# Optimization experiments

Hardware: AMD Instinct MI355X
Metric: run time of the kernel (lower is better)

The kernel has to match this reference:

```python
import jax, jax.numpy as jnp
import numpy as np

B = 131072
HID = 512
TEMB = 32
N_STEPS = 10


def time_embedding(t):
    # t: (B,) -> (B, TEMB) sinusoidal embedding
    half = TEMB // 2
    freqs = jnp.exp(-jnp.log(10000.0) * jnp.arange(half, dtype=jnp.float32) / half)
    args = t[:, None] * freqs[None, :]
    return jnp.concatenate([jnp.sin(args), jnp.cos(args)], axis=-1)


def setup_inputs() -> dict:
    key = jax.random.key(0)
    ks = jax.random.split(key, 9)
    def lin(k, fan_out, fan_in):
        s = 1.0 / np.sqrt(fan_in)
        kw, kb = jax.random.split(k)
        W = jax.random.uniform(kw, (fan_out, fan_in), jnp.float32, -s, s)
        b = jax.random.uniform(kb, (fan_out,), jnp.float32, -s, s)
        return W, b
    x = jax.random.normal(ks[0], (B, 2), jnp.float32)
    W0, b0 = lin(ks[1], HID, 2 + TEMB)
    W1, b1 = lin(ks[2], HID, HID)
    W2, b2 = lin(ks[3], HID, HID)
    # NOTE: original zero-inits last layer (trivial flow); use small random
    # weights so the Jacobian/log-det math is exercised non-trivially.
    W3 = 0.1 * jax.random.normal(ks[4], (2, HID), jnp.float32) / np.sqrt(HID)
    b3 = jnp.zeros((2,), jnp.float32)
    return {"x": x, "W0": W0, "b0": b0, "W1": W1, "b1": b1,
            "W2": W2, "b2": b2, "W3": W3, "b3": b3}


def reference(x, W0, b0, W1, b1, W2, b2, W3, b3):
    h_step = 1.0 / N_STEPS
    nb = x.shape[0]

    def vel(z, t):
        # z: (B,2), t: (B,) -> v: (B,2)
        h = jnp.concatenate([z, time_embedding(t)], axis=-1)
        h = jax.nn.silu(h @ W0.T + b0)
        h = jax.nn.silu(h @ W1.T + b1)
        h = jax.nn.silu(h @ W2.T + b2)
        return h @ W3.T + b3

    e0 = jnp.broadcast_to(jnp.array([1.0, 0.0], jnp.float32), (nb, 2))
    e1 = jnp.broadcast_to(jnp.array([0.0, 1.0], jnp.float32), (nb, 2))

    def step(carry, k):
        z, log_det = carry
        t = jnp.full((nb,), k * h_step, jnp.float32)
        f = lambda zz: vel(zz, t)
        # Batched JVPs give Jacobian columns: col0 = dv/dz0, col1 = dv/dz1
        v, col0 = jax.jvp(f, (z,), (e0,))
        _, col1 = jax.jvp(f, (z,), (e1,))
        det = (1.0 + h_step * col0[:, 0]) * (1.0 + h_step * col1[:, 1]) \
              - (h_step ** 2) * col1[:, 0] * col0[:, 1]
        log_det = log_det + jnp.log(jnp.clip(jnp.abs(det), 1e-8))
        z = z + h_step * v
        return (z, log_det), None

    ks = jnp.arange(N_STEPS, dtype=jnp.float32)
    (z, log_det), _ = jax.lax.scan(step, (x, jnp.zeros((nb,), jnp.float32)), ks)
    log_pz = -0.5 * jnp.sum(z ** 2 + jnp.log(2.0 * jnp.pi), axis=-1)
    return log_pz + log_det
```

## Files before the change

### kernel.cpp

```cpp
#include <hip/hip_runtime.h>
#include <hip/hip_bf16.h>
#include <math.h>


typedef float  f32x4  __attribute__((ext_vector_type(4)));
typedef float  f32x16 __attribute__((ext_vector_type(16)));
typedef __bf16 bf16x8 __attribute__((ext_vector_type(8)));

#define ROWB(r) (((r) << 10) + ((r) << 4))

static __device__ __forceinline__ unsigned pkbf2(float a, float b) {
    unsigned short lo = __builtin_bit_cast(unsigned short, __float2bfloat16(a));
    unsigned short hi = __builtin_bit_cast(unsigned short, __float2bfloat16(b));
    return (unsigned)lo | ((unsigned)hi << 16);
}

__global__ void pack_w_kernel(const float* __restrict__ W,
                              __hip_bfloat16* __restrict__ out) {
    int i  = blockIdx.x * 512 + threadIdx.x;
    int c  = i >> 13;
    int nb = (i >> 9) & 15;
    int l  = (i >> 3) & 63;
    int j  = i & 7;
    int n  = nb * 32 + (l & 31);
    int k  = c * 16 + ((l >> 5) << 3) + j;
    out[i] = __float2bfloat16(W[n * 512 + k]);
}

__global__ void pack_w0_kernel(const float* __restrict__ W0,
                               float* __restrict__ w01) {
    int o = threadIdx.x;
    w01[o * 2 + 0] = W0[o * 34 + 0];
    w01[o * 2 + 1] = W0[o * 34 + 1];
}

__global__ void cstep_kernel(const float* __restrict__ W0,
                             const float* __restrict__ b0,
                             float* __restrict__ cst) {
    int k = blockIdx.x;
    int o = threadIdx.x;
    float t = (float)k * 0.1f;
    float acc = b0[o];
    #pragma unroll
    for (int j = 0; j < 16; ++j) {
        float f   = expf(-9.210340371976184f * (float)j / 16.0f);
        float arg = t * f;
        acc += W0[o * 34 + 2 + j]  * sinf(arg);
        acc += W0[o * 34 + 18 + j] * cosf(arg);
    }
    cst[k * 512 + o] = acc;
}

__global__ __launch_bounds__(512)
void flow_kernel(const float* __restrict__ x,
                 const float* __restrict__ w01,
                 const float* __restrict__ cst,
                 const __hip_bfloat16* __restrict__ Wpk1,
                 const __hip_bfloat16* __restrict__ Wpk2,
                 const float* __restrict__ b1,
                 const float* __restrict__ b2,
                 const float* __restrict__ W3,
                 const float* __restrict__ b3v,
                 float* __restrict__ out)
{
    __shared__ __align__(16) char Xbuf[96 * 1040];
    __shared__ float zbuf[32][2];
    __shared__ float ldbuf[32];
    __shared__ __align__(16) float part[8][32][8];

    const int tid  = threadIdx.x;
    const int lane = tid & 63;
    const int wid  = tid >> 6;
    const int l31  = lane & 31;
    const int hi   = lane >> 5;
    const int n0w  = wid << 6;
    const int wgs  = blockIdx.x << 5;

    if (tid < 32) {
        zbuf[tid][0] = x[(wgs + tid) * 2 + 0];
        zbuf[tid][1] = x[(wgs + tid) * 2 + 1];
        ldbuf[tid]   = 0.0f;
    }

    const int rowb0 = ROWB(l31);
    const int rowb1 = ROWB(32 + l31);
    const int rowb2 = ROWB(64 + l31);
    const int hi16  = hi << 4;
    const int abase = (wid << 7) + lane;
    const uint4* Wp1 = (const uint4*)Wpk1;
    const uint4* Wp2 = (const uint4*)Wpk2;

    const int s0  = tid >> 4;
    const int t16 = tid & 15;

    const char* xb = (const char*)Xbuf;

    __syncthreads();

    #pragma unroll 1
    for (int step = 0; step < 10; ++step) {
        {
            const float z0 = zbuf[s0][0];
            const float z1 = zbuf[s0][1];
            const float* cs = cst + (step << 9);
            char* base0 = Xbuf + ROWB(s0);
            #pragma unroll 1
            for (int m = 0; m < 4; ++m) {
                int ob = (t16 << 5) + (m << 3);
                const float4* wv4 = (const float4*)(w01 + (ob << 1));
                const float4* cv4 = (const float4*)(cs + ob);
                unsigned ph[4], p0[4], p1[4];
                #pragma unroll
                for (int jj = 0; jj < 4; ++jj) {
                    float4 wv = wv4[jj];
                    float4 cv = cv4[jj >> 1];
                    float c0 = (jj & 1) ? cv.z : cv.x;
                    float c1 = (jj & 1) ? cv.w : cv.y;
                    float a0  = fmaf(z0, wv.x, fmaf(z1, wv.y, c0));
                    float sg0 = 1.0f / (1.0f + __expf(-a0));
                    float h0  = a0 * sg0;
                    float sp0 = fmaf(h0, 1.0f - sg0, sg0);
                    float a1  = fmaf(z0, wv.z, fmaf(z1, wv.w, c1));
                    float sg1 = 1.0f / (1.0f + __expf(-a1));
                    float h1  = a1 * sg1;
                    float sp1 = fmaf(h1, 1.0f - sg1, sg1);
                    ph[jj] = pkbf2(h0, h1);
                    p0[jj] = pkbf2(sp0 * wv.x, sp1 * wv.z);
                    p1[jj] = pkbf2(sp0 * wv.y, sp1 * wv.w);
                }
                int off = ob << 1;
                uint4 vph = {ph[0], ph[1], ph[2], ph[3]};
                uint4 vp0 = {p0[0], p0[1], p0[2], p0[3]};
                uint4 vp1 = {p1[0], p1[1], p1[2], p1[3]};
                *(uint4*)(base0 + off)             = vph;
                *(uint4*)(base0 + ROWB(32) + off)  = vp0;
                *(uint4*)(base0 + ROWB(64) + off)  = vp1;
            }
        }
        __syncthreads();

        #pragma unroll 1
        for (int layer = 0; layer < 2; ++layer) {
            const uint4* __restrict__ Wp   = layer ? Wp2 : Wp1;
            const float* __restrict__ bias = layer ? b2  : b1;

            f32x16 acc00 = (f32x16)(0.0f), acc01 = (f32x16)(0.0f), acc02 = (f32x16)(0.0f);
            f32x16 acc10 = (f32x16)(0.0f), acc11 = (f32x16)(0.0f), acc12 = (f32x16)(0.0f);

            uint4 aCur0 = Wp[abase];
            uint4 aCur1 = Wp[abase + 64];
            #pragma unroll 2
            for (int c = 0; c < 32; ++c) {
                int nidx = abase + (((c + 1) & 31) << 10);
                uint4 aNxt0 = Wp[nidx];
                uint4 aNxt1 = Wp[nidx + 64];
                int kx = (c << 5) | hi16;
                bf16x8 bf0 = __builtin_bit_cast(bf16x8, *(const uint4*)(xb + rowb0 + kx));
                bf16x8 bf1 = __builtin_bit_cast(bf16x8, *(const uint4*)(xb + rowb1 + kx));
                bf16x8 bf2 = __builtin_bit_cast(bf16x8, *(const uint4*)(xb + rowb2 + kx));
                bf16x8 av0 = __builtin_bit_cast(bf16x8, aCur0);
                bf16x8 av1 = __builtin_bit_cast(bf16x8, aCur1);
                __builtin_amdgcn_s_setprio(1);
                acc00 = __builtin_amdgcn_mfma_f32_32x32x16_bf16(av0, bf0, acc00, 0, 0, 0);
                acc10 = __builtin_amdgcn_mfma_f32_32x32x16_bf16(av1, bf0, acc10, 0, 0, 0);
                acc01 = __builtin_amdgcn_mfma_f32_32x32x16_bf16(av0, bf1, acc01, 0, 0, 0);
                acc11 = __builtin_amdgcn_mfma_f32_32x32x16_bf16(av1, bf1, acc11, 0, 0, 0);
                acc02 = __builtin_amdgcn_mfma_f32_32x32x16_bf16(av0, bf2, acc02, 0, 0, 0);
                acc12 = __builtin_amdgcn_mfma_f32_32x32x16_bf16(av1, bf2, acc12, 0, 0, 0);
                __builtin_amdgcn_s_setprio(0);
                aCur0 = aNxt0;
                aCur1 = aNxt1;
            }

            if (layer == 0) {
                __syncthreads();
                char* pb = Xbuf + ROWB(l31);
                #pragma unroll
                for (int nt = 0; nt < 2; ++nt) {
                    const f32x16& a0r = nt ? acc10 : acc00;
                    const f32x16& a1r = nt ? acc11 : acc01;
                    const f32x16& a2r = nt ? acc12 : acc02;
                    #pragma unroll
                    for (int q = 0; q < 4; ++q) {
                        int nq = n0w + nt * 32 + 8 * q + 4 * hi;
                        f32x4 bq = *(const f32x4*)(bias + nq);
                        float hv[4], u0v[4], u1v[4];
                        #pragma unroll
                        for (int k = 0; k < 4; ++k) {
                            int reg = 4 * q + k;
                            float aa  = a0r[reg] + bq[k];
                            float sig = 1.0f / (1.0f + __expf(-aa));
                            float h   = aa * sig;
                            float sp  = fmaf(h, 1.0f - sig, sig);
                            hv[k]  = h;
                            u0v[k] = sp * a1r[reg];
                            u1v[k] = sp * a2r[reg];
                        }
                        int off = nq << 1;
                        uint2 vh = {pkbf2(hv[0],  hv[1]),  pkbf2(hv[2],  hv[3])};
                        uint2 v0 = {pkbf2(u0v[0], u0v[1]), pkbf2(u0v[2], u0v[3])};
                        uint2 v1 = {pkbf2(u1v[0], u1v[1]), pkbf2(u1v[2], u1v[3])};
                        *(uint2*)(pb + off)            = vh;
                        *(uint2*)(pb + ROWB(32) + off) = v0;
                        *(uint2*)(pb + ROWB(64) + off) = v1;
                    }
                }
                __syncthreads();
            } else {
                float q0 = 0.f, q1 = 0.f, q2 = 0.f, q3 = 0.f, q4 = 0.f, q5 = 0.f;
                #pragma unroll
                for (int nt = 0; nt < 2; ++nt) {
                    const f32x16& a0r = nt ? acc10 : acc00;
                    const f32x16& a1r = nt ? acc11 : acc01;
                    const f32x16& a2r = nt ? acc12 : acc02;
                    #pragma unroll
                    for (int q = 0; q < 4; ++q) {
                        int nq = n0w + nt * 32 + 8 * q + 4 * hi;
                        f32x4 bq = *(const f32x4*)(bias + nq);
                        f32x4 w0 = *(const f32x4*)(W3 + nq);
                        f32x4 w1 = *(const f32x4*)(W3 + 512 + nq);
                        #pragma unroll
                        for (int k = 0; k < 4; ++k) {
                            int reg = 4 * q + k;
                            float aa  = a0r[reg] + bq[k];
                            float sig = 1.0f / (1.0f + __expf(-aa));
                            float h   = aa * sig;
                            float sp  = fmaf(h, 1.0f - sig, sig);
                            float u0  = sp * a1r[reg];
                            float u1  = sp * a2r[reg];
                            q0 = fmaf(w0[k], h,  q0);
                            q1 = fmaf(w1[k], h,  q1);
                            q2 = fmaf(w0[k], u0, q2);
                            q3 = fmaf(w1[k], u0, q3);
                            q4 = fmaf(w0[k], u1, q4);
                            q5 = fmaf(w1[k], u1, q5);
                        }
                    }
                }
                q0 += __shfl_xor(q0, 32);
                q1 += __shfl_xor(q1, 32);
                q2 += __shfl_xor(q2, 32);
                q3 += __shfl_xor(q3, 32);
                q4 += __shfl_xor(q4, 32);
                q5 += __shfl_xor(q5, 32);
                if (hi == 0) {
                    float* pp = &part[wid][l31][0];
                    pp[0] = q0; pp[1] = q1; pp[2] = q2;
                    pp[3] = q3; pp[4] = q4; pp[5] = q5;
                }
                __syncthreads();
            }
        }

        if (tid < 32) {
            float s0v = 0.f, s1v = 0.f, s2v = 0.f, s3v = 0.f, s4v = 0.f, s5v = 0.f;
            #pragma unroll
            for (int w = 0; w < 8; ++w) {
                const float* pp = &part[w][tid][0];
                f32x4 a = *(const f32x4*)(pp);
                f32x4 b = *(const f32x4*)(pp + 4);
                s0v += a[0]; s1v += a[1]; s2v += a[2];
                s3v += a[3]; s4v += b[0]; s5v += b[1];
            }
            float v0 = s0v + b3v[0];
            float v1 = s1v + b3v[1];
            float det = (1.0f + 0.1f * s2v) * (1.0f + 0.1f * s5v)
                      - 0.01f * s4v * s3v;
            ldbuf[tid] += logf(fmaxf(fabsf(det), 1e-8f));
            zbuf[tid][0] += 0.1f * v0;
            zbuf[tid][1] += 0.1f * v1;
        }
        __syncthreads();
    }

    if (tid < 32) {
        float z0 = zbuf[tid][0], z1 = zbuf[tid][1];
        out[wgs + tid] = -0.5f * (z0 * z0 + z1 * z1) - 1.8378770664093453f + ldbuf[tid];
    }
}

extern "C" void kernel_launch(void* const* d_in, const int* in_sizes, int n_in,
                              void* d_out, int out_size, void* d_ws, size_t ws_size,
                              hipStream_t stream) {
    const float* x  = (const float*)d_in[0];
    const float* W0 = (const float*)d_in[1];
    const float* b0 = (const float*)d_in[2];
    const float* W1 = (const float*)d_in[3];
    const float* b1 = (const float*)d_in[4];
    const float* W2 = (const float*)d_in[5];
    const float* b2 = (const float*)d_in[6];
    const float* W3 = (const float*)d_in[7];
    const float* b3 = (const float*)d_in[8];
    float* out = (float*)d_out;

    char* ws = (char*)d_ws;
    __hip_bfloat16* wpk1 = (__hip_bfloat16*)ws;
    __hip_bfloat16* wpk2 = (__hip_bfloat16*)(ws + (512u << 10));
    float*          cstp = (float*)(ws + (1024u << 10));
    float*          w01p = (float*)(ws + (1044u << 10));

    pack_w_kernel<<<512, 512, 0, stream>>>(W1, wpk1);
    pack_w_kernel<<<512, 512, 0, stream>>>(W2, wpk2);
    cstep_kernel<<<10, 512, 0, stream>>>(W0, b0, cstp);
    pack_w0_kernel<<<1, 512, 0, stream>>>(W0, w01p);
    flow_kernel<<<131072 / 32, 512, 0, stream>>>(x, w01p, cstp, wpk1, wpk2,
                                                 b1, b2, W3, b3, out);
}
```

Measured before the change: 4.951 ms.

## Keep flow state in registers redundantly, drop per-step barrier, deepen weight prefetch

Each thread now keeps its row's z and log-det in registers and redundantly performs the final per-row reduction over the partial sums. This removes the shared zbuf/ldbuf state, the serial 32-thread tail and the barrier at the end of every step. The partial-sum array is padded to 9 floats to reduce LDS bank conflicts, and the weight-fragment global prefetch is deepened from one to two iterations ahead. The cost is redundant reduction work in all threads and higher register pressure from the extra prefetch registers.

```diff
diff --git a/kernel.cpp b/kernel.cpp
--- a/kernel.cpp
+++ b/kernel.cpp
@@ -64,9 +64,7 @@
                  float* __restrict__ out)
 {
     __shared__ __align__(16) char Xbuf[96 * 1040];
-    __shared__ float zbuf[32][2];
-    __shared__ float ldbuf[32];
-    __shared__ __align__(16) float part[8][32][8];
+    __shared__ __align__(16) float part[8][32][9];
 
     const int tid  = threadIdx.x;
     const int lane = tid & 63;
@@ -76,12 +74,6 @@
     const int n0w  = wid << 6;
     const int wgs  = blockIdx.x << 5;
 
-    if (tid < 32) {
-        zbuf[tid][0] = x[(wgs + tid) * 2 + 0];
-        zbuf[tid][1] = x[(wgs + tid) * 2 + 1];
-        ldbuf[tid]   = 0.0f;
-    }
-
     const int rowb0 = ROWB(l31);
     const int rowb1 = ROWB(32 + l31);
     const int rowb2 = ROWB(64 + l31);
@@ -93,15 +85,17 @@
     const int s0  = tid >> 4;
     const int t16 = tid & 15;
 
+    float z0r = x[(wgs + s0) * 2 + 0];
+    float z1r = x[(wgs + s0) * 2 + 1];
+    float ldr = 0.0f;
+    const float b3x = b3v[0];
+    const float b3y = b3v[1];
+
     const char* xb = (const char*)Xbuf;
-
-    __syncthreads();
 
     #pragma unroll 1
     for (int step = 0; step < 10; ++step) {
         {
-            const float z0 = zbuf[s0][0];
-            const float z1 = zbuf[s0][1];
             const float* cs = cst + (step << 9);
             char* base0 = Xbuf + ROWB(s0);
             #pragma unroll 1
@@ -116,11 +110,11 @@
                     float4 cv = cv4[jj >> 1];
                     float c0 = (jj & 1) ? cv.z : cv.x;
                     float c1 = (jj & 1) ? cv.w : cv.y;
-                    float a0  = fmaf(z0, wv.x, fmaf(z1, wv.y, c0));
+                    float a0  = fmaf(z0r, wv.x, fmaf(z1r, wv.y, c0));
                     float sg0 = 1.0f / (1.0f + __expf(-a0));
                     float h0  = a0 * sg0;
                     float sp0 = fmaf(h0, 1.0f - sg0, sg0);
-                    float a1  = fmaf(z0, wv.z, fmaf(z1, wv.w, c1));
+                    float a1  = fmaf(z0r, wv.z, fmaf(z1r, wv.w, c1));
                     float sg1 = 1.0f / (1.0f + __expf(-a1));
                     float h1  = a1 * sg1;
                     float sp1 = fmaf(h1, 1.0f - sg1, sg1);
@@ -147,19 +141,21 @@
             f32x16 acc00 = (f32x16)(0.0f), acc01 = (f32x16)(0.0f), acc02 = (f32x16)(0.0f);
             f32x16 acc10 = (f32x16)(0.0f), acc11 = (f32x16)(0.0f), acc12 = (f32x16)(0.0f);
 
-            uint4 aCur0 = Wp[abase];
-            uint4 aCur1 = Wp[abase + 64];
+            uint4 aC0 = Wp[abase];
+            uint4 aC1 = Wp[abase + 64];
+            uint4 aN0 = Wp[abase + 1024];
+            uint4 aN1 = Wp[abase + 1024 + 64];
             #pragma unroll 2
             for (int c = 0; c < 32; ++c) {
-                int nidx = abase + (((c + 1) & 31) << 10);
-                uint4 aNxt0 = Wp[nidx];
-                uint4 aNxt1 = Wp[nidx + 64];
+                int i2 = abase + (((c + 2) & 31) << 10);
+                uint4 aF0 = Wp[i2];
+                uint4 aF1 = Wp[i2 + 64];
                 int kx = (c << 5) | hi16;
                 bf16x8 bf0 = __builtin_bit_cast(bf16x8, *(const uint4*)(xb + rowb0 + kx));
                 bf16x8 bf1 = __builtin_bit_cast(bf16x8, *(const uint4*)(xb + rowb1 + kx));
                 bf16x8 bf2 = __builtin_bit_cast(bf16x8, *(const uint4*)(xb + rowb2 + kx));
-                bf16x8 av0 = __builtin_bit_cast(bf16x8, aCur0);
-                bf16x8 av1 = __builtin_bit_cast(bf16x8, aCur1);
+                bf16x8 av0 = __builtin_bit_cast(bf16x8, aC0);
+                bf16x8 av1 = __builtin_bit_cast(bf16x8, aC1);
                 __builtin_amdgcn_s_setprio(1);
                 acc00 = __builtin_amdgcn_mfma_f32_32x32x16_bf16(av0, bf0, acc00, 0, 0, 0);
                 acc10 = __builtin_amdgcn_mfma_f32_32x32x16_bf16(av1, bf0, acc10, 0, 0, 0);
@@ -168,8 +164,8 @@
                 acc02 = __builtin_amdgcn_mfma_f32_32x32x16_bf16(av0, bf2, acc02, 0, 0, 0);
                 acc12 = __builtin_amdgcn_mfma_f32_32x32x16_bf16(av1, bf2, acc12, 0, 0, 0);
                 __builtin_amdgcn_s_setprio(0);
-                aCur0 = aNxt0;
-                aCur1 = aNxt1;
+                aC0 = aN0; aC1 = aN1;
+                aN0 = aF0; aN1 = aF1;
             }
 
             if (layer == 0) {
@@ -252,30 +248,26 @@
             }
         }
 
-        if (tid < 32) {
+        {
             float s0v = 0.f, s1v = 0.f, s2v = 0.f, s3v = 0.f, s4v = 0.f, s5v = 0.f;
             #pragma unroll
             for (int w = 0; w < 8; ++w) {
-                const float* pp = &part[w][tid][0];
-                f32x4 a = *(const f32x4*)(pp);
-                f32x4 b = *(const f32x4*)(pp + 4);
-                s0v += a[0]; s1v += a[1]; s2v += a[2];
-                s3v += a[3]; s4v += b[0]; s5v += b[1];
+                const float* pp = &part[w][s0][0];
+                s0v += pp[0]; s1v += pp[1]; s2v += pp[2];
+                s3v += pp[3]; s4v += pp[4]; s5v += pp[5];
             }
-            float v0 = s0v + b3v[0];
-            float v1 = s1v + b3v[1];
+            float v0 = s0v + b3x;
+            float v1 = s1v + b3y;
             float det = (1.0f + 0.1f * s2v) * (1.0f + 0.1f * s5v)
                       - 0.01f * s4v * s3v;
-            ldbuf[tid] += logf(fmaxf(fabsf(det), 1e-8f));
-            zbuf[tid][0] += 0.1f * v0;
-            zbuf[tid][1] += 0.1f * v1;
+            ldr += logf(fmaxf(fabsf(det), 1e-8f));
+            z0r += 0.1f * v0;
+            z1r += 0.1f * v1;
         }
-        __syncthreads();
     }
 
-    if (tid < 32) {
-        float z0 = zbuf[tid][0], z1 = zbuf[tid][1];
-        out[wgs + tid] = -0.5f * (z0 * z0 + z1 * z1) - 1.8378770664093453f + ldbuf[tid];
+    if (t16 == 0) {
+        out[wgs + s0] = -0.5f * (z0r * z0r + z1r * z1r) - 1.8378770664093453f + ldr;
     }
 }
 
```

Measured after the change: 5.154 ms. 4.1% more time.
